# Optimization experiments

Hardware: AMD Instinct MI355X
Metric: run time of the kernel (lower is better)

Reference implementation:

```python
import jax, jax.numpy as jnp
import numpy as np

N_NODES = 40000
N_EDGES = 640000
IN_CH = 128
HID1, HID2 = 512, 256
OUT_CH = 2
NUM_GRAPHS = 16
EPS = 1e-5


def layer_norm(x, g, b):
    mu = jnp.mean(x, axis=-1, keepdims=True)
    var = jnp.mean(jnp.square(x - mu), axis=-1, keepdims=True)
    return (x - mu) * jax.lax.rsqrt(var + EPS) * g + b


def gcn_conv(x, src, dst, ew, W, b, n_nodes):
    # PyG GCNConv: x' = x @ W; symmetric normalization with self-loops already
    # appended to (src, dst, ew) by the caller; bias added after aggregation.
    xw = x @ W                                            # [N, out]
    deg = jax.ops.segment_sum(ew, dst, num_segments=n_nodes)
    dinv = jnp.where(deg > 0, jax.lax.rsqrt(deg), 0.0)    # deg^{-1/2}, 0 for isolated
    norm = dinv[src] * ew * dinv[dst]                     # [E+N]
    msgs = norm[:, None] * xw[src]                        # gather + scale
    out = jax.ops.segment_sum(msgs, dst, num_segments=n_nodes)
    return out + b


def setup_inputs() -> dict:
    key = jax.random.key(0)
    ks = jax.random.split(key, 12)
    x = jax.random.normal(ks[0], (N_NODES, IN_CH), dtype=jnp.float32)
    edge_index = jax.random.randint(ks[1], (2, N_EDGES), 0, N_NODES, dtype=jnp.int64)
    edge_weight = jax.random.uniform(ks[2], (N_EDGES,), dtype=jnp.float32)
    batch = jnp.sort(jax.random.randint(ks[3], (N_NODES,), 0, NUM_GRAPHS, dtype=jnp.int64))
    # parameters (Glorot-ish scale)
    W1 = jax.random.normal(ks[4], (IN_CH, HID1), dtype=jnp.float32) / np.sqrt(IN_CH)
    b1 = jnp.zeros((HID1,), dtype=jnp.float32)
    g1 = jnp.ones((HID1,), dtype=jnp.float32)
    be1 = jnp.zeros((HID1,), dtype=jnp.float32)
    W2 = jax.random.normal(ks[5], (HID1, HID2), dtype=jnp.float32) / np.sqrt(HID1)
    b2 = jnp.zeros((HID2,), dtype=jnp.float32)
    g2 = jnp.ones((HID2,), dtype=jnp.float32)
    be2 = jnp.zeros((HID2,), dtype=jnp.float32)
    Wfc = jax.random.normal(ks[6], (HID2, OUT_CH), dtype=jnp.float32) / np.sqrt(HID2)
    bfc = jnp.zeros((OUT_CH,), dtype=jnp.float32)
    return {"x": x, "edge_index": edge_index, "edge_weight": edge_weight,
            "batch": batch, "W1": W1, "b1": b1, "g1": g1, "be1": be1,
            "W2": W2, "b2": b2, "g2": g2, "be2": be2, "Wfc": Wfc, "bfc": bfc}


def reference(x, edge_index, edge_weight, batch, W1, b1, g1, be1, W2, b2, g2, be2, Wfc, bfc):
    n = x.shape[0]
    loop = jnp.arange(n, dtype=edge_index.dtype)
    src = jnp.concatenate([edge_index[0], loop])
    dst = jnp.concatenate([edge_index[1], loop])
    ew = jnp.concatenate([edge_weight, jnp.ones((n,), dtype=edge_weight.dtype)])

    h = gcn_conv(x, src, dst, ew, W1, b1, n)
    h = layer_norm(jax.nn.relu(h), g1, be1)          # dropout = identity (eval)
    h3 = gcn_conv(h, src, dst, ew, W2, b2, n)
    h3 = layer_norm(jax.nn.relu(h3), g2, be2)

    # global mean pool over graph ids
    sums = jax.ops.segment_sum(h3, batch, num_segments=NUM_GRAPHS)
    cnts = jax.ops.segment_sum(jnp.ones((n,), dtype=h3.dtype), batch, num_segments=NUM_GRAPHS)
    pooled = sums / jnp.maximum(cnts, 1.0)[:, None]
    out = pooled @ Wfc + bfc
    return h3, out
```

## Files before the change

### kernel.cpp

```cpp
#include <hip/hip_runtime.h>
#include <hip/hip_bf16.h>

#define N_NODES   40000
#define N_EDGES   640000
#define IN_CH     128
#define HID1      512
#define HID2      256
#define OUT_CH    2
#define NUM_GRAPHS 16
#define EPSF      1e-5f
#define SCAN_NB   157
#define FIXSC     1048576.0f

typedef unsigned short u16;
typedef unsigned int   u32;
typedef unsigned long long u64;
using short8 = __attribute__((ext_vector_type(8))) short;
using f32x4  = __attribute__((ext_vector_type(4))) float;

__device__ __forceinline__ float b2f(u16 u) {
    return __uint_as_float(((u32)u) << 16);
}
__device__ __forceinline__ u16 f2b(float f) {
    u32 u = __float_as_uint(f);
    u32 r = (u + 0x7FFFu + ((u >> 16) & 1u)) >> 16;
    return (u16)r;
}
__device__ __forceinline__ void gload_lds16(const u16* g, u16* l) {
    __builtin_amdgcn_global_load_lds((const __attribute__((address_space(1))) u32*)g,
                                     (__attribute__((address_space(3))) u32*)l, 16, 0, 0);
}

__global__ __launch_bounds__(256) void packprep_kernel(const int* __restrict__ dst,
                                                       const float* __restrict__ ew,
                                                       u64* __restrict__ packed,
                                                       int* __restrict__ eoff,
                                                       const float* __restrict__ x,
                                                       u16* __restrict__ xb,
                                                       const float* __restrict__ W1,
                                                       u16* __restrict__ W1T,
                                                       const float* __restrict__ W2,
                                                       u16* __restrict__ W2T) {
    int t = blockIdx.x * blockDim.x + threadIdx.x;
    if (t < N_EDGES) {
        int d = dst[t];
        u64 inc = (1ull << 40) | (u64)__float2uint_rn(ew[t] * FIXSC);
        u64 old = atomicAdd(&packed[d], inc);
        eoff[t] = (int)(old >> 40);
    }
    if (t < N_NODES * IN_CH / 4) {
        float4 v = ((const float4*)x)[t];
        ushort4 o = { f2b(v.x), f2b(v.y), f2b(v.z), f2b(v.w) };
        ((ushort4*)xb)[t] = o;
    }
    if (t < IN_CH * HID1) {
        int r = t / HID1, c = t % HID1;
        W1T[(size_t)c * IN_CH + r] = f2b(W1[t]);
    }
    if (t < HID1 * HID2) {
        int r = t / HID2, c = t % HID2;
        W2T[(size_t)c * HID1 + r] = f2b(W2[t]);
    }
}

__global__ __launch_bounds__(256) void scan_p1_kernel(const u64* __restrict__ packed,
                                                      float* __restrict__ dinv,
                                                      int* __restrict__ rowptr,
                                                      int* __restrict__ blocksum) {
    __shared__ int sd[256];
    const int t = threadIdx.x;
    const int i = blockIdx.x * 256 + t;
    int v = 0;
    if (i < N_NODES) {
        u64 p = packed[i];
        v = (int)(p >> 40);
        float deg = (float)(p & ((1ull << 40) - 1)) * (1.0f / FIXSC);
        dinv[i] = rsqrtf(deg + 1.0f);
    }
    sd[t] = v;
    __syncthreads();
    for (int off = 1; off < 256; off <<= 1) {
        int u = (t >= off) ? sd[t - off] : 0;
        __syncthreads();
        sd[t] += u;
        __syncthreads();
    }
    if (i < N_NODES) rowptr[i] = sd[t] - v;
    if (t == 255) blocksum[blockIdx.x] = sd[255];
}

__global__ __launch_bounds__(256) void scan_p2_kernel(int* __restrict__ blocksum,
                                                      int* __restrict__ bprefix,
                                                      const int* __restrict__ batch,
                                                      int* __restrict__ gstart) {
    __shared__ int sd[256];
    const int t = threadIdx.x;
    const int v = (t < SCAN_NB) ? blocksum[t] : 0;
    sd[t] = v;
    __syncthreads();
    for (int off = 1; off < 256; off <<= 1) {
        int u = (t >= off) ? sd[t - off] : 0;
        __syncthreads();
        sd[t] += u;
        __syncthreads();
    }
    bprefix[t] = sd[t] - v;
    if (t <= NUM_GRAPHS) {
        int lo = 0, hi = N_NODES;
        while (lo < hi) {
            int mid = (lo + hi) >> 1;
            if (batch[mid] < t) lo = mid + 1; else hi = mid;
        }
        gstart[t] = lo;
    }
}

__global__ __launch_bounds__(256) void scan_p3_kernel(int* __restrict__ rowptr,
                                                      const int* __restrict__ bprefix) {
    const int i = blockIdx.x * 256 + threadIdx.x;
    if (i < N_NODES) rowptr[i] += bprefix[blockIdx.x];
    if (i == 0) rowptr[N_NODES] = N_EDGES;
}

__global__ __launch_bounds__(256) void scatter_kernel(const int* __restrict__ src,
                                                      const int* __restrict__ dst,
                                                      const float* __restrict__ ew,
                                                      const float* __restrict__ dinv,
                                                      const int* __restrict__ rowptr,
                                                      const int* __restrict__ eoff,
                                                      int2* __restrict__ csr_pair) {
    int t = blockIdx.x * blockDim.x + threadIdx.x;
    if (t >= N_EDGES) return;
    int s = src[t], d = dst[t];
    int pos = rowptr[d] + eoff[t];
    float norm = dinv[s] * ew[t] * dinv[d];
    int2 pr; pr.x = s; pr.y = __float_as_int(norm);
    csr_pair[pos] = pr;
}

__global__ __launch_bounds__(256) void agg128_kernel(const int* __restrict__ rowptr,
                                                     const int2* __restrict__ csr_pair,
                                                     const float* __restrict__ dinv,
                                                     const u16* __restrict__ xb,
                                                     u16* __restrict__ outb) {
    const int node = (blockIdx.x * blockDim.x + threadIdx.x) >> 6;
    const int l = threadIdx.x & 63;
    if (node >= N_NODES) return;
    const int half = l >> 5, cl = l & 31;
    const float ds = dinv[node];
    const float wself = half ? 0.f : ds * ds;
    const int e0 = rowptr[node], e1 = rowptr[node + 1];
    const int c0 = cl * 4;

    ushort4 sv = *(const ushort4*)&xb[(size_t)node * IN_CH + c0];
    float acc[4] = { wself * b2f(sv.x), wself * b2f(sv.y),
                     wself * b2f(sv.z), wself * b2f(sv.w) };
    int e = e0;
    for (; e + 8 <= e1; e += 8) {
        int2 p[4]; ushort4 u[4];
#pragma unroll
        for (int j = 0; j < 4; ++j) p[j] = csr_pair[e + half + 2 * j];
#pragma unroll
        for (int j = 0; j < 4; ++j) u[j] = *(const ushort4*)&xb[(size_t)p[j].x * IN_CH + c0];
#pragma unroll
        for (int j = 0; j < 4; ++j) {
            float w = __int_as_float(p[j].y);
            acc[0] += w * b2f(u[j].x);
            acc[1] += w * b2f(u[j].y);
            acc[2] += w * b2f(u[j].z);
            acc[3] += w * b2f(u[j].w);
        }
    }
    for (int ee = e + half; ee < e1; ee += 2) {
        int2 p = csr_pair[ee];
        float w = __int_as_float(p.y);
        ushort4 u = *(const ushort4*)&xb[(size_t)p.x * IN_CH + c0];
        acc[0] += w * b2f(u.x);
        acc[1] += w * b2f(u.y);
        acc[2] += w * b2f(u.z);
        acc[3] += w * b2f(u.w);
    }
#pragma unroll
    for (int j = 0; j < 4; ++j) acc[j] += __shfl_xor(acc[j], 32);
    float a0 = half ? acc[2] : acc[0];
    float a1 = half ? acc[3] : acc[1];
    ushort2 o = { f2b(a0), f2b(a1) };
    *(ushort2*)&outb[(size_t)node * IN_CH + c0 + half * 2] = o;
}

__global__ __launch_bounds__(256) void agg256_ln_kernel(const int* __restrict__ rowptr,
                                                        const int2* __restrict__ csr_pair,
                                                        const float* __restrict__ dinv,
                                                        const u16* __restrict__ hwb,
                                                        const float* __restrict__ bias,
                                                        const float* __restrict__ g,
                                                        const float* __restrict__ be,
                                                        float* __restrict__ out) {
    const int node = (blockIdx.x * blockDim.x + threadIdx.x) >> 6;
    const int l = threadIdx.x & 63;
    if (node >= N_NODES) return;
    const int half = l >> 5, cl = l & 31;
    const float ds = dinv[node];
    const float wself = half ? 0.f : ds * ds;
    const int e0 = rowptr[node], e1 = rowptr[node + 1];
    const int c0 = cl * 8;

    short8 sv = *(const short8*)&hwb[(size_t)node * HID2 + c0];
    float acc[8];
#pragma unroll
    for (int j = 0; j < 8; ++j) acc[j] = wself * b2f((u16)sv[j]);

    int e = e0;
    for (; e + 8 <= e1; e += 8) {
        int2 p[4]; short8 u[4];
#pragma unroll
        for (int j = 0; j < 4; ++j) p[j] = csr_pair[e + half + 2 * j];
#pragma unroll
        for (int j = 0; j < 4; ++j) u[j] = *(const short8*)&hwb[(size_t)p[j].x * HID2 + c0];
#pragma unroll
        for (int j = 0; j < 4; ++j) {
            float w = __int_as_float(p[j].y);
#pragma unroll
            for (int k = 0; k < 8; ++k) acc[k] += w * b2f((u16)u[j][k]);
        }
    }
    for (int ee = e + half; ee < e1; ee += 2) {
        int2 p = csr_pair[ee];
        float w = __int_as_float(p.y);
        short8 u = *(const short8*)&hwb[(size_t)p.x * HID2 + c0];
#pragma unroll
        for (int k = 0; k < 8; ++k) acc[k] += w * b2f((u16)u[k]);
    }
#pragma unroll
    for (int j = 0; j < 8; ++j) acc[j] += __shfl_xor(acc[j], 32);

    float4 blo = *(const float4*)&bias[c0];
    float4 bhi = *(const float4*)&bias[c0 + 4];
    float vv[8];
    float sum = 0.f, sq = 0.f;
#pragma unroll
    for (int j = 0; j < 8; ++j) {
        float bj = (j < 4) ? ((const float*)&blo)[j] : ((const float*)&bhi)[j - 4];
        float xv = fmaxf(acc[j] + bj, 0.f);
        vv[j] = xv;
        sum += xv;
        sq += xv * xv;
    }
#pragma unroll
    for (int off = 1; off <= 16; off <<= 1) {
        sum += __shfl_xor(sum, off);
        sq  += __shfl_xor(sq, off);
    }
    const float mean = sum * (1.0f / HID2);
    const float var = sq * (1.0f / HID2) - mean * mean;
    const float r = rsqrtf(var + EPSF);

    const int cw = c0 + half * 4;
    float4 gq = *(const float4*)&g[cw];
    float4 bq = *(const float4*)&be[cw];
    float s0 = half ? vv[4] : vv[0];
    float s1 = half ? vv[5] : vv[1];
    float s2 = half ? vv[6] : vv[2];
    float s3 = half ? vv[7] : vv[3];
    float4 o;
    o.x = (s0 - mean) * r * gq.x + bq.x;
    o.y = (s1 - mean) * r * gq.y + bq.y;
    o.z = (s2 - mean) * r * gq.z + bq.z;
    o.w = (s3 - mean) * r * gq.w + bq.w;
    *(float4*)&out[(size_t)node * HID2 + cw] = o;
}

__global__ __launch_bounds__(512) void gemm1ln_kernel(const u16* __restrict__ A,
                                                      const u16* __restrict__ BT,
                                                      const float* __restrict__ b1,
                                                      const float* __restrict__ g1,
                                                      const float* __restrict__ be1,
                                                      u16* __restrict__ H) {
    __shared__ u16 As[64 * 32];
    __shared__ u16 Bs[512 * 32];
    __shared__ float lsum[8][64];
    __shared__ float lsq[8][64];
    __shared__ float lmean[64];
    __shared__ float lrstd[64];
    const int t = threadIdx.x;
    const int l = t & 63;
    const int wv = t >> 6;
    const int fr = l & 15;
    const int fg = l >> 4;
    const int rowbase = blockIdx.x * 64;

    f32x4 acc[4][4];
#pragma unroll
    for (int a = 0; a < 4; ++a)
#pragma unroll
        for (int b = 0; b < 4; ++b)
            acc[a][b] = (f32x4){0.f, 0.f, 0.f, 0.f};

    for (int k0 = 0; k0 < IN_CH; k0 += 32) {
        if (t < 256)
            gload_lds16(A + (size_t)(rowbase + (t >> 2)) * IN_CH + k0 + (t & 3) * 8,
                        As + t * 8);
#pragma unroll
        for (int j = 0; j < 4; ++j) {
            int c = t + 512 * j;
            gload_lds16(BT + (size_t)(c >> 2) * IN_CH + k0 + (c & 3) * 8,
                        Bs + c * 8);
        }
        __syncthreads();

        short8 af[4], bf[4];
#pragma unroll
        for (int fm = 0; fm < 4; ++fm)
            af[fm] = *(const short8*)&As[(fm * 16 + fr) * 32 + fg * 8];
#pragma unroll
        for (int fn = 0; fn < 4; ++fn)
            bf[fn] = *(const short8*)&Bs[(wv * 64 + fn * 16 + fr) * 32 + fg * 8];
#pragma unroll
        for (int fm = 0; fm < 4; ++fm)
#pragma unroll
            for (int fn = 0; fn < 4; ++fn)
                acc[fm][fn] = __builtin_amdgcn_mfma_f32_16x16x32_bf16(af[fm], bf[fn], acc[fm][fn], 0, 0, 0);
        __syncthreads();
    }

    const int colb = wv * 64;
    float bc[4], gc[4], bec[4];
#pragma unroll
    for (int fn = 0; fn < 4; ++fn) {
        int col = colb + fn * 16 + fr;
        bc[fn] = b1[col];
        gc[fn] = g1[col];
        bec[fn] = be1[col];
    }
    float ps[4][4], pq[4][4];
#pragma unroll
    for (int fm = 0; fm < 4; ++fm)
#pragma unroll
        for (int i = 0; i < 4; ++i) { ps[fm][i] = 0.f; pq[fm][i] = 0.f; }
#pragma unroll
    for (int fm = 0; fm < 4; ++fm)
#pragma unroll
        for (int fn = 0; fn < 4; ++fn)
#pragma unroll
            for (int i = 0; i < 4; ++i) {
                float xv = fmaxf(acc[fm][fn][i] + bc[fn], 0.f);
                acc[fm][fn][i] = xv;
                ps[fm][i] += xv;
                pq[fm][i] += xv * xv;
            }
#pragma unroll
    for (int off = 1; off < 16; off <<= 1)
#pragma unroll
        for (int fm = 0; fm < 4; ++fm)
#pragma unroll
            for (int i = 0; i < 4; ++i) {
                ps[fm][i] += __shfl_xor(ps[fm][i], off);
                pq[fm][i] += __shfl_xor(pq[fm][i], off);
            }
    if (fr == 0) {
#pragma unroll
        for (int fm = 0; fm < 4; ++fm)
#pragma unroll
            for (int i = 0; i < 4; ++i) {
                int row = fm * 16 + fg * 4 + i;
                lsum[wv][row] = ps[fm][i];
                lsq[wv][row] = pq[fm][i];
            }
    }
    __syncthreads();
    if (t < 64) {
        float s = 0.f, q = 0.f;
#pragma unroll
        for (int w = 0; w < 8; ++w) { s += lsum[w][t]; q += lsq[w][t]; }
        float mean = s * (1.0f / HID1);
        float var = q * (1.0f / HID1) - mean * mean;
        lmean[t] = mean;
        lrstd[t] = rsqrtf(var + EPSF);
    }
    __syncthreads();
#pragma unroll
    for (int fm = 0; fm < 4; ++fm)
#pragma unroll
        for (int fn = 0; fn < 4; ++fn)
#pragma unroll
            for (int i = 0; i < 4; ++i) {
                int row = fm * 16 + fg * 4 + i;
                int col = colb + fn * 16 + fr;
                float o = (acc[fm][fn][i] - lmean[row]) * lrstd[row] * gc[fn] + bec[fn];
                H[(size_t)(rowbase + row) * HID1 + col] = f2b(o);
            }
}

__global__ __launch_bounds__(512) void gemm2_kernel(const u16* __restrict__ A,
                                                    const u16* __restrict__ BT,
                                                    u16* __restrict__ Cb) {
    __shared__ u16 As[128 * 32];
    __shared__ u16 Bs[256 * 32];
    const int t = threadIdx.x;
    const int l = t & 63;
    const int wv = t >> 6;
    const int wm = (wv >> 2) * 64;
    const int wn = (wv & 3) * 64;
    const int fr = l & 15;
    const int fg = l >> 4;
    const int rowbase = blockIdx.x * 128;

    f32x4 acc[4][4];
#pragma unroll
    for (int a = 0; a < 4; ++a)
#pragma unroll
        for (int b = 0; b < 4; ++b)
            acc[a][b] = (f32x4){0.f, 0.f, 0.f, 0.f};

    int ar = rowbase + (t >> 2); if (ar >= N_NODES) ar = N_NODES - 1;
    const u16* ag = A + (size_t)ar * HID1 + (t & 3) * 8;
    const int cb0 = t, cb1 = t + 512;
    const u16* bg0 = BT + (size_t)(cb0 >> 2) * HID1 + (cb0 & 3) * 8;
    const u16* bg1 = BT + (size_t)(cb1 >> 2) * HID1 + (cb1 & 3) * 8;

    for (int k0 = 0; k0 < HID1; k0 += 32) {
        gload_lds16(ag + k0, As + t * 8);
        gload_lds16(bg0 + k0, Bs + cb0 * 8);
        gload_lds16(bg1 + k0, Bs + cb1 * 8);
        __syncthreads();

        short8 af[4], bf[4];
#pragma unroll
        for (int fm = 0; fm < 4; ++fm)
            af[fm] = *(const short8*)&As[(wm + fm * 16 + fr) * 32 + fg * 8];
#pragma unroll
        for (int fn = 0; fn < 4; ++fn)
            bf[fn] = *(const short8*)&Bs[(wn + fn * 16 + fr) * 32 + fg * 8];
#pragma unroll
        for (int fm = 0; fm < 4; ++fm)
#pragma unroll
            for (int fn = 0; fn < 4; ++fn)
                acc[fm][fn] = __builtin_amdgcn_mfma_f32_16x16x32_bf16(af[fm], bf[fn], acc[fm][fn], 0, 0, 0);
        __syncthreads();
    }

#pragma unroll
    for (int fm = 0; fm < 4; ++fm)
#pragma unroll
        for (int fn = 0; fn < 4; ++fn) {
#pragma unroll
            for (int i = 0; i < 4; ++i) {
                int row = rowbase + wm + fm * 16 + fg * 4 + i;
                if (row < N_NODES) {
                    int col = wn + fn * 16 + fr;
                    Cb[(size_t)row * HID2 + col] = f2b(acc[fm][fn][i]);
                }
            }
        }
}

__global__ __launch_bounds__(256) void pool2_kernel(const float* __restrict__ h3,
                                                    const int* __restrict__ gstart,
                                                    float* __restrict__ part) {
    const int g = blockIdx.x, chunk = blockIdx.y;
    const int s = gstart[g], e = gstart[g + 1];
    const int len = e - s;
    const int c0 = s + (len * chunk) / 16;
    const int c1 = s + (len * (chunk + 1)) / 16;
    float acc = 0.f;
    for (int n = c0; n < c1; ++n)
        acc += h3[(size_t)n * HID2 + threadIdx.x];
    part[(size_t)(g * 16 + chunk) * HID2 + threadIdx.x] = acc;
}

__global__ __launch_bounds__(256) void fc_kernel(const float* __restrict__ part,
                                                 const int* __restrict__ gstart,
                                                 const float* __restrict__ Wfc,
                                                 const float* __restrict__ bfc,
                                                 float* __restrict__ out) {
    __shared__ float r0[256], r1[256];
    const int t = threadIdx.x;
    const float w0 = Wfc[t * 2], w1 = Wfc[t * 2 + 1];
    for (int g = 0; g < NUM_GRAPHS; ++g) {
        float v = 0.f;
#pragma unroll
        for (int k = 0; k < 16; ++k)
            v += part[(size_t)(g * 16 + k) * HID2 + t];
        r0[t] = v * w0;
        r1[t] = v * w1;
        __syncthreads();
        for (int off = 128; off >= 1; off >>= 1) {
            if (t < off) { r0[t] += r0[t + off]; r1[t] += r1[t + off]; }
            __syncthreads();
        }
        if (t == 0) {
            float inv = 1.0f / fmaxf((float)(gstart[g + 1] - gstart[g]), 1.0f);
            out[g * 2 + 0] = r0[0] * inv + bfc[0];
            out[g * 2 + 1] = r1[0] * inv + bfc[1];
        }
        __syncthreads();
    }
}

extern "C" void kernel_launch(void* const* d_in, const int* in_sizes, int n_in,
                              void* d_out, int out_size, void* d_ws, size_t ws_size,
                              hipStream_t stream) {
    const float* x   = (const float*)d_in[0];
    const int*   ei  = (const int*)d_in[1];
    const float* ew  = (const float*)d_in[2];
    const int*   bat = (const int*)d_in[3];
    const float* W1  = (const float*)d_in[4];
    const float* b1  = (const float*)d_in[5];
    const float* g1  = (const float*)d_in[6];
    const float* be1 = (const float*)d_in[7];
    const float* W2  = (const float*)d_in[8];
    const float* b2  = (const float*)d_in[9];
    const float* g2  = (const float*)d_in[10];
    const float* be2 = (const float*)d_in[11];
    const float* Wfc = (const float*)d_in[12];
    const float* bfc = (const float*)d_in[13];

    const int* srcArr = ei;
    const int* dstArr = ei + N_EDGES;

    float* out = (float*)d_out;
    float* h3  = out;
    float* fcO = out + (size_t)N_NODES * HID2;

    float* ws       = (float*)d_ws;
    u64*   packed   = (u64*)ws;
    float* dinv     = ws + 81920;
    int*   rowptr   = (int*)(ws + 122880);
    int*   gstart   = (int*)(ws + 163968);
    int*   blocksum = (int*)(ws + 164032);
    int*   bprefix  = (int*)(ws + 164288);
    int*   eoff     = (int*)(ws + 164544);
    int2*  csr_pair = (int2*)(ws + 804544);
    u16*   xb       = (u16*)(ws + 2084544);
    u16*   agg1b    = (u16*)(ws + 4644544);
    u16*   hb       = (u16*)(ws + 7204544);
    u16*   hwb      = (u16*)(ws + 17444544);
    u16*   W1T      = (u16*)(ws + 22564544);
    u16*   W2T      = (u16*)(ws + 22597312);
    float* part     = ws + 22662848;

    hipMemsetAsync(packed, 0, 40960 * sizeof(u64), stream);
    packprep_kernel<<<(N_NODES * IN_CH / 4 + 255) / 256, 256, 0, stream>>>(
        dstArr, ew, packed, eoff, x, xb, W1, W1T, W2, W2T);

    scan_p1_kernel<<<SCAN_NB, 256, 0, stream>>>(packed, dinv, rowptr, blocksum);
    scan_p2_kernel<<<1, 256, 0, stream>>>(blocksum, bprefix, bat, gstart);
    scan_p3_kernel<<<SCAN_NB, 256, 0, stream>>>(rowptr, bprefix);
    scatter_kernel<<<(N_EDGES + 255) / 256, 256, 0, stream>>>(
        srcArr, dstArr, ew, dinv, rowptr, eoff, csr_pair);

    agg128_kernel<<<(N_NODES + 3) / 4, 256, 0, stream>>>(
        rowptr, csr_pair, dinv, xb, agg1b);
    gemm1ln_kernel<<<N_NODES / 64, 512, 0, stream>>>(agg1b, W1T, b1, g1, be1, hb);

    gemm2_kernel<<<(N_NODES + 127) / 128, 512, 0, stream>>>(hb, W2T, hwb);
    agg256_ln_kernel<<<(N_NODES + 3) / 4, 256, 0, stream>>>(
        rowptr, csr_pair, dinv, hwb, b2, g2, be2, h3);

    {
        dim3 grid(NUM_GRAPHS, 16);
        pool2_kernel<<<grid, 256, 0, stream>>>(h3, gstart, part);
    }
    fc_kernel<<<1, 256, 0, stream>>>(part, gstart, Wfc, bfc, fcO);
}
```

Measured before the change: 258.8 us.

## Split layer-2 aggregation into column-sliced blocks and separate ReLU+LayerNorm pass

Replaces the fused per-node 256-wide aggregation+LayerNorm kernel with a kernel that processes 32-column slices per block (8 slices, block index interleaved), with 8 lanes per edge group handling 8 edges in parallel. The aim is that blocks working on the same column slice share a smaller L2 working set for gathered rows and expose more edge-level parallelism. ReLU/bias/LayerNorm moves into a separate kernel that re-reads and rewrites h3 in fp32. This costs an extra kernel launch and an extra full read/write of the 40000x256 fp32 output, and each node's row pointers and edge list are now read 8 times.

```diff
diff --git a/kernel.cpp b/kernel.cpp
--- a/kernel.cpp
+++ b/kernel.cpp
@@ -188,86 +188,96 @@
     *(ushort2*)&outb[(size_t)node * IN_CH + c0 + half * 2] = o;
 }
 
-__global__ __launch_bounds__(256) void agg256_ln_kernel(const int* __restrict__ rowptr,
-                                                        const int2* __restrict__ csr_pair,
-                                                        const float* __restrict__ dinv,
-                                                        const u16* __restrict__ hwb,
-                                                        const float* __restrict__ bias,
-                                                        const float* __restrict__ g,
-                                                        const float* __restrict__ be,
-                                                        float* __restrict__ out) {
-    const int node = (blockIdx.x * blockDim.x + threadIdx.x) >> 6;
+__global__ __launch_bounds__(256) void agg256_slice_kernel(const int* __restrict__ rowptr,
+                                                           const int2* __restrict__ csr_pair,
+                                                           const float* __restrict__ dinv,
+                                                           const u16* __restrict__ hwb,
+                                                           float* __restrict__ out) {
+    const int bid = blockIdx.x;
+    const int s = bid & 7;
+    const int node = ((bid >> 3) << 2) + (threadIdx.x >> 6);
     const int l = threadIdx.x & 63;
     if (node >= N_NODES) return;
-    const int half = l >> 5, cl = l & 31;
-    const float ds = dinv[node];
-    const float wself = half ? 0.f : ds * ds;
+    const int eg = l >> 3, li = l & 7;
+    const int c0 = s * 32 + li * 4;
     const int e0 = rowptr[node], e1 = rowptr[node + 1];
-    const int c0 = cl * 8;
-
-    short8 sv = *(const short8*)&hwb[(size_t)node * HID2 + c0];
-    float acc[8];
-#pragma unroll
-    for (int j = 0; j < 8; ++j) acc[j] = wself * b2f((u16)sv[j]);
-
+
+    float a0 = 0.f, a1 = 0.f, a2 = 0.f, a3 = 0.f;
+    if (eg == 0) {
+        float ds = dinv[node];
+        float wself = ds * ds;
+        ushort4 sv = *(const ushort4*)&hwb[(size_t)node * HID2 + c0];
+        a0 = wself * b2f(sv.x); a1 = wself * b2f(sv.y);
+        a2 = wself * b2f(sv.z); a3 = wself * b2f(sv.w);
+    }
     int e = e0;
-    for (; e + 8 <= e1; e += 8) {
-        int2 p[4]; short8 u[4];
-#pragma unroll
-        for (int j = 0; j < 4; ++j) p[j] = csr_pair[e + half + 2 * j];
-#pragma unroll
-        for (int j = 0; j < 4; ++j) u[j] = *(const short8*)&hwb[(size_t)p[j].x * HID2 + c0];
-#pragma unroll
-        for (int j = 0; j < 4; ++j) {
-            float w = __int_as_float(p[j].y);
-#pragma unroll
-            for (int k = 0; k < 8; ++k) acc[k] += w * b2f((u16)u[j][k]);
-        }
-    }
-    for (int ee = e + half; ee < e1; ee += 2) {
-        int2 p = csr_pair[ee];
-        float w = __int_as_float(p.y);
-        short8 u = *(const short8*)&hwb[(size_t)p.x * HID2 + c0];
-#pragma unroll
-        for (int k = 0; k < 8; ++k) acc[k] += w * b2f((u16)u[k]);
-    }
-#pragma unroll
-    for (int j = 0; j < 8; ++j) acc[j] += __shfl_xor(acc[j], 32);
-
-    float4 blo = *(const float4*)&bias[c0];
-    float4 bhi = *(const float4*)&bias[c0 + 4];
-    float vv[8];
-    float sum = 0.f, sq = 0.f;
-#pragma unroll
-    for (int j = 0; j < 8; ++j) {
-        float bj = (j < 4) ? ((const float*)&blo)[j] : ((const float*)&bhi)[j - 4];
-        float xv = fmaxf(acc[j] + bj, 0.f);
-        vv[j] = xv;
-        sum += xv;
-        sq += xv * xv;
-    }
-#pragma unroll
-    for (int off = 1; off <= 16; off <<= 1) {
+    for (; e + 16 <= e1; e += 16) {
+        int2 p0 = csr_pair[e + eg];
+        int2 p1 = csr_pair[e + 8 + eg];
+        ushort4 u0 = *(const ushort4*)&hwb[(size_t)p0.x * HID2 + c0];
+        ushort4 u1 = *(const ushort4*)&hwb[(size_t)p1.x * HID2 + c0];
+        float w0 = __int_as_float(p0.y), w1 = __int_as_float(p1.y);
+        a0 += w0 * b2f(u0.x) + w1 * b2f(u1.x);
+        a1 += w0 * b2f(u0.y) + w1 * b2f(u1.y);
+        a2 += w0 * b2f(u0.z) + w1 * b2f(u1.z);
+        a3 += w0 * b2f(u0.w) + w1 * b2f(u1.w);
+    }
+    for (; e < e1; e += 8) {
+        int ee = e + eg;
+        float w = 0.f; int src = 0;
+        if (ee < e1) { int2 p = csr_pair[ee]; src = p.x; w = __int_as_float(p.y); }
+        ushort4 u = *(const ushort4*)&hwb[(size_t)src * HID2 + c0];
+        a0 += w * b2f(u.x);
+        a1 += w * b2f(u.y);
+        a2 += w * b2f(u.z);
+        a3 += w * b2f(u.w);
+    }
+#pragma unroll
+    for (int off = 8; off <= 32; off <<= 1) {
+        a0 += __shfl_xor(a0, off);
+        a1 += __shfl_xor(a1, off);
+        a2 += __shfl_xor(a2, off);
+        a3 += __shfl_xor(a3, off);
+    }
+    if (l < 8) {
+        float4 o = { a0, a1, a2, a3 };
+        *(float4*)&out[(size_t)node * HID2 + s * 32 + l * 4] = o;
+    }
+}
+
+__global__ __launch_bounds__(256) void relu_ln256_kernel(float* __restrict__ io,
+                                                         const float* __restrict__ bias,
+                                                         const float* __restrict__ g,
+                                                         const float* __restrict__ be) {
+    const int wv = (blockIdx.x * blockDim.x + threadIdx.x) >> 6;
+    const int lane = threadIdx.x & 63;
+    if (wv >= N_NODES) return;
+    float* __restrict__ row = io + (size_t)wv * HID2;
+    const int c0 = lane * 4;
+    float4 a = *(const float4*)&row[c0];
+    float4 bq = *(const float4*)&bias[c0];
+    float v0 = fmaxf(a.x + bq.x, 0.f);
+    float v1 = fmaxf(a.y + bq.y, 0.f);
+    float v2 = fmaxf(a.z + bq.z, 0.f);
+    float v3 = fmaxf(a.w + bq.w, 0.f);
+    float sum = v0 + v1 + v2 + v3;
+    float sq = v0 * v0 + v1 * v1 + v2 * v2 + v3 * v3;
+#pragma unroll
+    for (int off = 32; off >= 1; off >>= 1) {
         sum += __shfl_xor(sum, off);
         sq  += __shfl_xor(sq, off);
     }
     const float mean = sum * (1.0f / HID2);
     const float var = sq * (1.0f / HID2) - mean * mean;
     const float r = rsqrtf(var + EPSF);
-
-    const int cw = c0 + half * 4;
-    float4 gq = *(const float4*)&g[cw];
-    float4 bq = *(const float4*)&be[cw];
-    float s0 = half ? vv[4] : vv[0];
-    float s1 = half ? vv[5] : vv[1];
-    float s2 = half ? vv[6] : vv[2];
-    float s3 = half ? vv[7] : vv[3];
+    float4 gq = *(const float4*)&g[c0];
+    float4 eq = *(const float4*)&be[c0];
     float4 o;
-    o.x = (s0 - mean) * r * gq.x + bq.x;
-    o.y = (s1 - mean) * r * gq.y + bq.y;
-    o.z = (s2 - mean) * r * gq.z + bq.z;
-    o.w = (s3 - mean) * r * gq.w + bq.w;
-    *(float4*)&out[(size_t)node * HID2 + cw] = o;
+    o.x = (v0 - mean) * r * gq.x + eq.x;
+    o.y = (v1 - mean) * r * gq.y + eq.y;
+    o.z = (v2 - mean) * r * gq.z + eq.z;
+    o.w = (v3 - mean) * r * gq.w + eq.w;
+    *(float4*)&row[c0] = o;
 }
 
 __global__ __launch_bounds__(512) void gemm1ln_kernel(const u16* __restrict__ A,
@@ -554,8 +564,9 @@
     gemm1ln_kernel<<<N_NODES / 64, 512, 0, stream>>>(agg1b, W1T, b1, g1, be1, hb);
 
     gemm2_kernel<<<(N_NODES + 127) / 128, 512, 0, stream>>>(hb, W2T, hwb);
-    agg256_ln_kernel<<<(N_NODES + 3) / 4, 256, 0, stream>>>(
-        rowptr, csr_pair, dinv, hwb, b2, g2, be2, h3);
+    agg256_slice_kernel<<<((N_NODES + 3) / 4) * 8, 256, 0, stream>>>(
+        rowptr, csr_pair, dinv, hwb, h3);
+    relu_ln256_kernel<<<(N_NODES + 3) / 4, 256, 0, stream>>>(h3, b2, g2, be2);
 
     {
         dim3 grid(NUM_GRAPHS, 16);
```

New measurement: 334.9 us. +29.4%, slower.
